# Optimization experiments

Hardware: AMD Instinct MI355X
Metric: run time of the kernel (lower is better)

Reference implementation:

```python
import jax, jax.numpy as jnp
import numpy as np

G = 32            # gridsize
N = G * G         # num_nodes = 1024
F_IN = 32         # input_dim
H = 256           # hidden_dim
L = 4             # n_layers
B = 64            # batch
MID = F_IN + L * H
MIN_VAL = -10000000.0
EPS_LN = 1e-5
EPS_BN = 1e-5


def _grid_edges():
    ids = np.arange(N).reshape(G, G)
    hs, hd = ids[:, :-1].ravel(), ids[:, 1:].ravel()
    vs, vd = ids[:-1, :].ravel(), ids[1:, :].ravel()
    src = np.concatenate([hs, hd, vs, vd]).astype(np.int32)
    dst = np.concatenate([hd, hs, vd, vs]).astype(np.int32)
    return jnp.asarray(src), jnp.asarray(dst)


def setup_inputs() -> dict:
    key = jax.random.key(0)
    ks = jax.random.split(key, 16)
    mask_f = jax.random.bernoulli(ks[0], 0.7, (B, N)).astype(jnp.float32)
    feats = jax.random.normal(ks[1], (B, N * F_IN), dtype=jnp.float32)
    observations = jnp.concatenate([mask_f, feats], axis=1)
    src, dst = _grid_edges()
    def lin(k, fi, fo):
        return jax.random.normal(k, (fi, fo), dtype=jnp.float32) / np.sqrt(fi)
    W0 = lin(ks[2], F_IN, H); b0 = jnp.zeros((H,), jnp.float32)
    g0 = jnp.ones((H,), jnp.float32); be0 = jnp.zeros((H,), jnp.float32)
    Ws = jax.random.normal(ks[3], (L - 1, H, H), jnp.float32) / np.sqrt(H)
    bs = jnp.zeros((L - 1, H), jnp.float32)
    gs = jnp.ones((L - 1, H), jnp.float32); bes = jnp.zeros((L - 1, H), jnp.float32)
    W1 = lin(ks[4], MID, 2 * H); b1 = jnp.zeros((2 * H,), jnp.float32)
    bn_g = jnp.ones((2 * H,), jnp.float32); bn_b = jnp.zeros((2 * H,), jnp.float32)
    bn_m = jax.random.normal(ks[5], (2 * H,), jnp.float32) * 0.1
    bn_v = jax.random.uniform(ks[6], (2 * H,), jnp.float32, 0.5, 1.5)
    W2 = lin(ks[7], 2 * H, 1); b2 = jnp.zeros((1,), jnp.float32)
    return {"observations": observations, "src": src, "dst": dst,
            "W0": W0, "b0": b0, "g0": g0, "be0": be0,
            "Ws": Ws, "bs": bs, "gs": gs, "bes": bes,
            "W1": W1, "b1": b1, "bn_g": bn_g, "bn_b": bn_b,
            "bn_m": bn_m, "bn_v": bn_v, "W2": W2, "b2": b2}


def _layer_norm(z, g, b):
    mu = z.mean(-1, keepdims=True)
    var = z.var(-1, keepdims=True)
    return (z - mu) / jnp.sqrt(var + EPS_LN) * g + b


def reference(observations, src, dst, W0, b0, g0, be0, Ws, bs, gs, bes,
              W1, b1, bn_g, bn_b, bn_m, bn_v, W2, b2):
    mask = observations[:, :N] != 0.0                      # [B,N] bool action mask
    x = observations[:, N:].reshape(B, N, F_IN)            # node features
    outs = [x]
    h = x
    for l in range(L):
        # GIN with eps=-1: (1+eps)*x_i vanishes -> mlp(sum of neighbor features)
        agg = jnp.zeros_like(h).at[:, dst, :].add(h[:, src, :])
        W, bb, g, be = ((W0, b0, g0, be0) if l == 0
                        else (Ws[l - 1], bs[l - 1], gs[l - 1], bes[l - 1]))
        h = jax.nn.relu(_layer_norm(agg @ W + bb, g, be))  # mlp ReLU; outer .relu() is idempotent
        outs.append(h)
    xc = jnp.concatenate(outs, axis=-1).reshape(B * N, MID)
    z = xc @ W1 + b1
    z = (z - bn_m) / jnp.sqrt(bn_v + EPS_BN) * bn_g + bn_b  # BatchNorm1d eval mode
    z = jax.nn.relu(z)                                       # dropout off in eval
    y = (z @ W2 + b2).reshape(B, N)
    return jnp.where(mask, y, MIN_VAL)
```

## Files before the change

kernel.cpp:

```cpp
#include <hip/hip_runtime.h>
#include <stdint.h>

#define FIN 32
#define HD 256
#define MIDK 1056
#define HF 512
#define MROWS 65536
#define OBS_STRIDE 33792

typedef float f32x2 __attribute__((ext_vector_type(2)));
typedef float f32x4 __attribute__((ext_vector_type(4)));


__device__ __forceinline__ unsigned pack4fp8(float a, float b, float c, float d) {
    int w = __builtin_amdgcn_cvt_pk_fp8_f32(a, b, 0, false);
    return (unsigned)__builtin_amdgcn_cvt_pk_fp8_f32(c, d, w, true);
}
__device__ __forceinline__ unsigned char f2fp8(float f) {
    return (unsigned char)(__builtin_amdgcn_cvt_pk_fp8_f32(f, f, 0, false) & 0xff);
}

__device__ __forceinline__ void glds16(const void* g, void* l) {
    __builtin_amdgcn_global_load_lds(
        (const __attribute__((address_space(1))) unsigned int*)g,
        (__attribute__((address_space(3))) unsigned int*)l,
        16, 0, 0);
}

#define WAITV(N) asm volatile("s_waitcnt vmcnt(" #N ")" ::: "memory")
#define WAITLGKM0() asm volatile("s_waitcnt lgkmcnt(0)" ::: "memory")
__device__ __forceinline__ void barx() {
    asm volatile("" ::: "memory");
    __builtin_amdgcn_s_barrier();
    asm volatile("" ::: "memory");
}

__device__ __forceinline__ void gather16(const float* __restrict__ src, int stride, int n,
                                         unsigned char* __restrict__ dst) {
    float f[16];
#pragma unroll
    for (int j = 0; j < 16; ++j) f[j] = src[(size_t)j * stride + n];
    uint4 o;
    o.x = pack4fp8(f[0],  f[1],  f[2],  f[3]);
    o.y = pack4fp8(f[4],  f[5],  f[6],  f[7]);
    o.z = pack4fp8(f[8],  f[9],  f[10], f[11]);
    o.w = pack4fp8(f[12], f[13], f[14], f[15]);
    *(uint4*)dst = o;
}

__global__ __launch_bounds__(256) void k_prep_w(
        const float* __restrict__ W0, const float* __restrict__ Ws,
        const float* __restrict__ W1,
        unsigned char* __restrict__ Wt0, unsigned char* __restrict__ WtL,
        unsigned char* __restrict__ WtF) {
    const int b = blockIdx.x, t = threadIdx.x;
    if (b < 2) {
        int s = b * 256 + t;
        int hh = s >> 8, n = s & 255;
        gather16(W0 + (size_t)(hh * 16) * HD, HD, n, Wt0 + (size_t)s * 16);
    } else if (b < 50) {
        int u = (b - 2) * 256 + t;
        int l = u >> 12, s = u & 4095;
        int kb = s >> 9, hh = (s >> 8) & 1, n = s & 255;
        gather16(Ws + (size_t)l * 65536 + (size_t)(kb * 32 + hh * 16) * HD, HD, n,
                 WtL + (size_t)l * 65536 + (size_t)s * 16);
    } else {
        int s = (b - 50) * 256 + t;
        int kb = s >> 11, hh = (s >> 9) & 3, n = s & 511;
        int k0 = kb * 64 + hh * 16;
        if (k0 < MIDK)
            gather16(W1 + (size_t)k0 * HF, HF, n, WtF + (size_t)s * 16);
        else
            *(uint4*)(WtF + (size_t)s * 16) = make_uint4(0, 0, 0, 0);
    }
}

template <int K>
__global__ __launch_bounds__(256, 4) void k_layer(
        const unsigned char* __restrict__ Hin,
        const float* __restrict__ obs,
        const unsigned char* __restrict__ Wt,
        const float* __restrict__ bias, const float* __restrict__ gamma,
        const float* __restrict__ beta, unsigned char* __restrict__ Hout) {
    constexpr int KB = K / 32;
    __shared__ __align__(16) unsigned char Agg[(K / 16) * 64 * 16];
    __shared__ float ls[64], lss[64];
    const int t = threadIdx.x;
    const int w = t >> 6, lane = t & 63, quad = lane >> 4, l15 = lane & 15;
    const int q1 = quad >> 1, q0 = quad & 1;
    const int m0 = ((blockIdx.x & 7) * 128 + (blockIdx.x >> 3)) * 64;
    const int img = m0 >> 10, node0 = m0 & 1023;
    if (t < 64) { ls[t] = 0.f; lss[t] = 0.f; }

    if constexpr (K == 256) {
        const int r = t & 63, sg = t >> 6;
        const int node = node0 + r;
        const int rr = node >> 5, cc = node & 31;
        const unsigned char* Hb = Hin + (size_t)img * 262144;
#pragma unroll
        for (int p = 0; p < 2; ++p) {
            const int seg = p * 4 + sg;
            float s[32];
#pragma unroll
            for (int i = 0; i < 32; ++i) s[i] = 0.f;
            auto addn = [&](int nn) {
                uint4 u0 = *(const uint4*)(Hb + ((size_t)(2 * seg) * 1024 + nn) * 16);
                uint4 u1 = *(const uint4*)(Hb + ((size_t)(2 * seg + 1) * 1024 + nn) * 16);
                unsigned uu[8] = {u0.x, u0.y, u0.z, u0.w, u1.x, u1.y, u1.z, u1.w};
#pragma unroll
                for (int i = 0; i < 8; ++i) {
                    f32x2 lo = __builtin_amdgcn_cvt_pk_f32_fp8(uu[i], false);
                    f32x2 hi = __builtin_amdgcn_cvt_pk_f32_fp8(uu[i], true);
                    s[4 * i + 0] += lo.x; s[4 * i + 1] += lo.y;
                    s[4 * i + 2] += hi.x; s[4 * i + 3] += hi.y;
                }
            };
            if (cc > 0)  addn(node - 1);
            if (cc < 31) addn(node + 1);
            if (rr > 0)  addn(node - 32);
            if (rr < 31) addn(node + 32);
            unsigned ow[8];
#pragma unroll
            for (int i = 0; i < 8; ++i)
                ow[i] = pack4fp8(s[4 * i], s[4 * i + 1], s[4 * i + 2], s[4 * i + 3]);
            ((uint4*)Agg)[(2 * seg) * 64 + r]     = make_uint4(ow[0], ow[1], ow[2], ow[3]);
            ((uint4*)Agg)[(2 * seg + 1) * 64 + r] = make_uint4(ow[4], ow[5], ow[6], ow[7]);
        }
    } else {
        const int r = t >> 2, seg4 = t & 3;
        const int node = node0 + r;
        const int rr = node >> 5, cc = node & 31;
        const float* fb = obs + (size_t)img * OBS_STRIDE + 1024 + seg4 * 8;
        float s[8] = {0, 0, 0, 0, 0, 0, 0, 0};
        auto addnf = [&](int nn) {
            const float4* fp = (const float4*)(fb + nn * 32);
            float4 f0 = fp[0], f1 = fp[1];
            s[0] += f0.x; s[1] += f0.y; s[2] += f0.z; s[3] += f0.w;
            s[4] += f1.x; s[5] += f1.y; s[6] += f1.z; s[7] += f1.w;
        };
        if (cc > 0)  addnf(node - 1);
        if (cc < 31) addnf(node + 1);
        if (rr > 0)  addnf(node - 32);
        if (rr < 31) addnf(node + 32);
        uint2 o;
        o.x = pack4fp8(s[0], s[1], s[2], s[3]);
        o.y = pack4fp8(s[4], s[5], s[6], s[7]);
        *(uint2*)(Agg + ((seg4 >> 1) * 64 + r) * 16 + (seg4 & 1) * 8) = o;
    }
    __syncthreads();

    f32x4 acc[4][4] = {};
    const unsigned char* bbase = Wt + ((size_t)(q1 * 256 + w * 64 + l15)) * 16 + q0 * 8;
    const unsigned char* abase = Agg + ((size_t)(q1 * 64 + l15)) * 16 + q0 * 8;

#define LOADBL(dst, kb) { const unsigned char* bp = bbase + (size_t)(kb) * 8192; \
    dst[0] = *(const long long*)(bp);        dst[1] = *(const long long*)(bp + 256); \
    dst[2] = *(const long long*)(bp + 512);  dst[3] = *(const long long*)(bp + 768); }
#define MFMAL(buf, kb) { long long af[4]; \
    _Pragma("unroll") for (int mt = 0; mt < 4; ++mt) \
        af[mt] = *(const long long*)(abase + (kb) * 2048 + mt * 256); \
    _Pragma("unroll") for (int mt = 0; mt < 4; ++mt) \
    _Pragma("unroll") for (int nt = 0; nt < 4; ++nt) \
        acc[mt][nt] = __builtin_amdgcn_mfma_f32_16x16x32_fp8_fp8(af[mt], buf[nt], acc[mt][nt], 0, 0, 0); }

    if constexpr (KB == 1) {
        long long bA[4];
        LOADBL(bA, 0);
        MFMAL(bA, 0);
    } else {
        long long bA[4], bB[4];
        LOADBL(bA, 0);
#pragma unroll
        for (int j = 0; j < KB / 2 - 1; ++j) {
            LOADBL(bB, 2 * j + 1);
            MFMAL(bA, 2 * j);
            LOADBL(bA, 2 * j + 2);
            MFMAL(bB, 2 * j + 1);
        }
        LOADBL(bB, KB - 1);
        MFMAL(bA, KB - 2);
        MFMAL(bB, KB - 1);
    }
#undef LOADBL
#undef MFMAL

#pragma unroll
    for (int mt = 0; mt < 4; ++mt) {
        float s0 = 0, s1 = 0, s2 = 0, s3 = 0, u0 = 0, u1 = 0, u2 = 0, u3 = 0;
#pragma unroll
        for (int nt = 0; nt < 4; ++nt) {
            int col = w * 64 + nt * 16 + l15;
            float bv = bias[col];
            f32x4 vv = acc[mt][nt];
            vv.x += bv; vv.y += bv; vv.z += bv; vv.w += bv;
            acc[mt][nt] = vv;
            s0 += vv.x; u0 += vv.x * vv.x;
            s1 += vv.y; u1 += vv.y * vv.y;
            s2 += vv.z; u2 += vv.z * vv.z;
            s3 += vv.w; u3 += vv.w * vv.w;
        }
#pragma unroll
        for (int msk = 1; msk < 16; msk <<= 1) {
            s0 += __shfl_xor(s0, msk); u0 += __shfl_xor(u0, msk);
            s1 += __shfl_xor(s1, msk); u1 += __shfl_xor(u1, msk);
            s2 += __shfl_xor(s2, msk); u2 += __shfl_xor(u2, msk);
            s3 += __shfl_xor(s3, msk); u3 += __shfl_xor(u3, msk);
        }
        if (l15 == 0) {
            int rl = mt * 16 + quad * 4;
            atomicAdd(&ls[rl + 0], s0); atomicAdd(&lss[rl + 0], u0);
            atomicAdd(&ls[rl + 1], s1); atomicAdd(&lss[rl + 1], u1);
            atomicAdd(&ls[rl + 2], s2); atomicAdd(&lss[rl + 2], u2);
            atomicAdd(&ls[rl + 3], s3); atomicAdd(&lss[rl + 3], u3);
        }
    }
    __syncthreads();
#pragma unroll
    for (int mt = 0; mt < 4; ++mt) {
        int rl = mt * 16 + quad * 4;
        float mu0 = ls[rl + 0] * (1.f / 256.f), mu1 = ls[rl + 1] * (1.f / 256.f);
        float mu2 = ls[rl + 2] * (1.f / 256.f), mu3 = ls[rl + 3] * (1.f / 256.f);
        float rs0 = rsqrtf(lss[rl + 0] * (1.f / 256.f) - mu0 * mu0 + 1e-5f);
        float rs1 = rsqrtf(lss[rl + 1] * (1.f / 256.f) - mu1 * mu1 + 1e-5f);
        float rs2 = rsqrtf(lss[rl + 2] * (1.f / 256.f) - mu2 * mu2 + 1e-5f);
        float rs3 = rsqrtf(lss[rl + 3] * (1.f / 256.f) - mu3 * mu3 + 1e-5f);
#pragma unroll
        for (int nt = 0; nt < 4; ++nt) {
            int col = w * 64 + nt * 16 + l15;
            float gg = gamma[col], be = beta[col];
            f32x4 vv = acc[mt][nt];
            size_t rb = ((size_t)(img * 16 + w * 4 + nt) * 1024
                         + node0 + mt * 16 + quad * 4) * 16 + l15;
            Hout[rb]      = f2fp8(fmaxf((vv.x - mu0) * rs0 * gg + be, 0.f));
            Hout[rb + 16] = f2fp8(fmaxf((vv.y - mu1) * rs1 * gg + be, 0.f));
            Hout[rb + 32] = f2fp8(fmaxf((vv.z - mu2) * rs2 * gg + be, 0.f));
            Hout[rb + 48] = f2fp8(fmaxf((vv.w - mu3) * rs3 * gg + be, 0.f));
        }
    }
}

__global__ __launch_bounds__(512) void k_final(
        const unsigned char* __restrict__ h0, const unsigned char* __restrict__ h1,
        const unsigned char* __restrict__ h2, const unsigned char* __restrict__ h3,
        const unsigned char* __restrict__ WtF,
        const float* __restrict__ b1,
        const float* __restrict__ bng, const float* __restrict__ bnb,
        const float* __restrict__ bnm, const float* __restrict__ bnv,
        const float* __restrict__ W2, const float* __restrict__ b2,
        const float* __restrict__ obs, float* __restrict__ out) {
    __shared__ __align__(16) unsigned char As[2][264 * 16];
    __shared__ __align__(16) unsigned char Bsm[2][2056 * 16];
    __shared__ float yred[64];
    const int t = threadIdx.x;
    const int w = t >> 6, lane = t & 63, quad = lane >> 4, l15 = lane & 15;
    const int q1 = quad >> 1, q0 = quad & 1;
    const int wr = w >> 2, wc = w & 3;
    const int m0 = ((blockIdx.x & 7) * 128 + (blockIdx.x >> 3)) * 64;
    const int bimg = m0 >> 10, node0 = m0 & 1023;
    if (t < 64) yred[t] = 0.f;

    const unsigned char* hbuf[4] = {h0, h1, h2, h3};
    f32x4 acc[2][8] = {};

    auto stageB = [&](int it, unsigned char* Bb, int nB) {
#pragma unroll
        for (int i = 0; i < nB; ++i)
            glds16(WtF + ((size_t)it * 2048 + (size_t)i * 512 + t) * 16,
                   Bb + ((size_t)i * 514 + (t & ~63)) * 16);
    };
    auto stageA = [&](int it, unsigned char* Ab, int steps) {
        if (t < steps * 128) {
            int h = t >> 6, r = t & 63;
            int j = it * 64 + h * 16 - FIN;
            glds16(hbuf[j >> 8] + ((size_t)(bimg * 16 + ((j & 255) >> 4)) * 1024 + node0 + r) * 16,
                   Ab + (size_t)h * 66 * 16);
        }
    };
    auto compute = [&](const unsigned char* Ab, const unsigned char* Bb, int steps) {
        for (int s2 = 0; s2 < steps; ++s2) {
            long long af[2], bf[8];
#pragma unroll
            for (int mt = 0; mt < 2; ++mt)
                af[mt] = *(const long long*)(Ab + ((s2 * 2 + q1) * 66 + wr * 32 + mt * 16 + l15) * 16 + q0 * 8);
#pragma unroll
            for (int nt = 0; nt < 8; ++nt)
                bf[nt] = *(const long long*)(Bb + ((size_t)((s2 * 2 + q1) * 514 + wc * 128 + nt * 16 + l15)) * 16 + q0 * 8);
            __builtin_amdgcn_s_setprio(1);
#pragma unroll
            for (int mt = 0; mt < 2; ++mt)
#pragma unroll
                for (int nt = 0; nt < 8; ++nt)
                    acc[mt][nt] = __builtin_amdgcn_mfma_f32_16x16x32_fp8_fp8(af[mt], bf[nt], acc[mt][nt], 0, 0, 0);
            __builtin_amdgcn_s_setprio(0);
        }
    };

    if (t < 128) {
        int h = t >> 6, r = t & 63;
        const float* p = obs + (size_t)bimg * OBS_STRIDE + 1024 + (node0 + r) * 32 + h * 16;
        float4 f0 = *(const float4*)p, f1 = *(const float4*)(p + 4);
        float4 f2 = *(const float4*)(p + 8), f3 = *(const float4*)(p + 12);
        uint4 o;
        o.x = pack4fp8(f0.x, f0.y, f0.z, f0.w);
        o.y = pack4fp8(f1.x, f1.y, f1.z, f1.w);
        o.z = pack4fp8(f2.x, f2.y, f2.z, f2.w);
        o.w = pack4fp8(f3.x, f3.y, f3.z, f3.w);
        *(uint4*)(As[0] + (h * 66 + r) * 16) = o;
    } else if (t < 256) {
        int h = t >> 6, r = t & 63;
        glds16(h0 + ((size_t)(bimg * 16 + (h - 2)) * 1024 + node0 + r) * 16,
               As[0] + (size_t)h * 66 * 16);
    }
    stageB(0, Bsm[0], 4);
    stageA(1, As[1], 2);
    stageB(1, Bsm[1], 4);
    if (w < 4) { WAITV(5); } else { WAITV(4); }
    WAITLGKM0();
    barx();
    compute(As[0], Bsm[0], 2);
    barx();

#pragma unroll 1
    for (int it = 1; it < 17; ++it) {
        const int cur = it & 1;
        if (it < 15) {
            stageA(it + 1, As[cur ^ 1], 2);
            stageB(it + 1, Bsm[cur ^ 1], 4);
            if (w < 4) { WAITV(5); } else { WAITV(4); }
        } else if (it == 15) {
            stageA(16, As[cur ^ 1], 1);
            stageB(16, Bsm[cur ^ 1], 2);
            if (w < 2) { WAITV(3); } else { WAITV(2); }
        } else {
            WAITV(0);
        }
        barx();
        compute(As[cur], Bsm[cur], (it < 16) ? 2 : 1);
        barx();
    }

    float scv[8], sbv[8], w2v[8];
#pragma unroll
    for (int nt = 0; nt < 8; ++nt) {
        int col = wc * 128 + nt * 16 + l15;
        float sc = bng[col] * rsqrtf(bnv[col] + 1e-5f);
        scv[nt] = sc;
        sbv[nt] = (b1[col] - bnm[col]) * sc + bnb[col];
        w2v[nt] = W2[col];
    }
#pragma unroll
    for (int mt = 0; mt < 2; ++mt) {
        float p0 = 0, p1 = 0, p2 = 0, p3 = 0;
#pragma unroll
        for (int nt = 0; nt < 8; ++nt) {
            f32x4 vv = acc[mt][nt];
            p0 += fmaxf(vv.x * scv[nt] + sbv[nt], 0.f) * w2v[nt];
            p1 += fmaxf(vv.y * scv[nt] + sbv[nt], 0.f) * w2v[nt];
            p2 += fmaxf(vv.z * scv[nt] + sbv[nt], 0.f) * w2v[nt];
            p3 += fmaxf(vv.w * scv[nt] + sbv[nt], 0.f) * w2v[nt];
        }
#pragma unroll
        for (int msk = 1; msk < 16; msk <<= 1) {
            p0 += __shfl_xor(p0, msk);
            p1 += __shfl_xor(p1, msk);
            p2 += __shfl_xor(p2, msk);
            p3 += __shfl_xor(p3, msk);
        }
        if (l15 == 0) {
            int rl = wr * 32 + mt * 16 + quad * 4;
            atomicAdd(&yred[rl + 0], p0);
            atomicAdd(&yred[rl + 1], p1);
            atomicAdd(&yred[rl + 2], p2);
            atomicAdd(&yred[rl + 3], p3);
        }
    }
    __syncthreads();
    if (t < 64) {
        int gm = m0 + t;
        float mk = obs[(size_t)bimg * OBS_STRIDE + (node0 + t)];
        out[gm] = (mk != 0.f) ? yred[t] + b2[0] : -10000000.0f;
    }
}

extern "C" void kernel_launch(void* const* d_in, const int* in_sizes, int n_in,
                              void* d_out, int out_size, void* d_ws, size_t ws_size,
                              hipStream_t stream) {
    const float* obs = (const float*)d_in[0];
    const float* W0  = (const float*)d_in[3];
    const float* b0  = (const float*)d_in[4];
    const float* g0  = (const float*)d_in[5];
    const float* be0 = (const float*)d_in[6];
    const float* Ws  = (const float*)d_in[7];
    const float* bs  = (const float*)d_in[8];
    const float* gs  = (const float*)d_in[9];
    const float* bes = (const float*)d_in[10];
    const float* W1  = (const float*)d_in[11];
    const float* b1  = (const float*)d_in[12];
    const float* bng = (const float*)d_in[13];
    const float* bnb = (const float*)d_in[14];
    const float* bnm = (const float*)d_in[15];
    const float* bnv = (const float*)d_in[16];
    const float* W2  = (const float*)d_in[17];
    const float* b2  = (const float*)d_in[18];
    float* out = (float*)d_out;

    char* ws = (char*)d_ws;
    unsigned char* h0  = (unsigned char*)(ws);
    unsigned char* h1  = (unsigned char*)(ws + 16777216);
    unsigned char* h2  = (unsigned char*)(ws + 33554432);
    unsigned char* h3  = (unsigned char*)(ws + 50331648);
    unsigned char* Wt0 = (unsigned char*)(ws + 67108864);
    unsigned char* WtL = (unsigned char*)(ws + 67117056);
    unsigned char* WtF = (unsigned char*)(ws + 67313664);

    k_prep_w<<<182, 256, 0, stream>>>(W0, Ws, W1, Wt0, WtL, WtF);

    k_layer<FIN><<<1024, 256, 0, stream>>>(h0 , obs, Wt0, b0, g0, be0, h0);
    k_layer<HD> <<<1024, 256, 0, stream>>>(h0, obs, WtL,              bs,       gs,       bes,       h1);
    k_layer<HD> <<<1024, 256, 0, stream>>>(h1, obs, WtL + 65536,      bs + 256, gs + 256, bes + 256, h2);
    k_layer<HD> <<<1024, 256, 0, stream>>>(h2, obs, WtL + 2 * 65536,  bs + 512, gs + 512, bes + 512, h3);

    k_final<<<1024, 512, 0, stream>>>(h0, h1, h2, h3, WtF, b1, bng, bnb, bnm, bnv,
                                      W2, b2, obs, out);
}
```

Baseline: 234.3 us.

## Use 16x16x128 scaled FP8 MFMA in final GEMM with 128-wide K stages

Moves the final 1056x512 projection from 16x16x32 fp8 MFMAs to the gfx950 scaled 16x16x128 f8f6f4 MFMA, with neutral scale exponents. The K pipeline now takes 128-wide steps (9 iterations instead of 17). Each wave owns all 64 rows and a 64-column slice instead of a 32x128 tile. The W1 pre-transpose layout and the prep grid size change to match. This cuts instruction issue and loop and barrier overhead, at the cost of larger LDS buffers and padded K (1056 to 1152), which means wasted MFMA work and possible LDS bank conflicts from removing the row padding.

```diff
diff --git a/kernel.cpp b/kernel.cpp
--- a/kernel.cpp
+++ b/kernel.cpp
@@ -10,6 +10,8 @@
 
 typedef float f32x2 __attribute__((ext_vector_type(2)));
 typedef float f32x4 __attribute__((ext_vector_type(4)));
+typedef int   i32x4 __attribute__((ext_vector_type(4)));
+typedef int   i32x8 __attribute__((ext_vector_type(8)));
 
 
 __device__ __forceinline__ unsigned pack4fp8(float a, float b, float c, float d) {
@@ -66,8 +68,9 @@
                  WtL + (size_t)l * 65536 + (size_t)s * 16);
     } else {
         int s = (b - 50) * 256 + t;
-        int kb = s >> 11, hh = (s >> 9) & 3, n = s & 511;
-        int k0 = kb * 64 + hh * 16;
+        int it = s >> 12, r2 = s & 4095;
+        int hh = r2 >> 9, n = r2 & 511;
+        int k0 = it * 128 + hh * 16;
         if (k0 < MIDK)
             gather16(W1 + (size_t)k0 * HF, HF, n, WtF + (size_t)s * 16);
         else
@@ -248,56 +251,61 @@
         const float* __restrict__ bnm, const float* __restrict__ bnv,
         const float* __restrict__ W2, const float* __restrict__ b2,
         const float* __restrict__ obs, float* __restrict__ out) {
-    __shared__ __align__(16) unsigned char As[2][264 * 16];
-    __shared__ __align__(16) unsigned char Bsm[2][2056 * 16];
+    __shared__ __align__(16) unsigned char As[2][8 * 64 * 16];
+    __shared__ __align__(16) unsigned char Bsm[2][8 * 512 * 16];
     __shared__ float yred[64];
     const int t = threadIdx.x;
     const int w = t >> 6, lane = t & 63, quad = lane >> 4, l15 = lane & 15;
-    const int q1 = quad >> 1, q0 = quad & 1;
-    const int wr = w >> 2, wc = w & 3;
     const int m0 = ((blockIdx.x & 7) * 128 + (blockIdx.x >> 3)) * 64;
     const int bimg = m0 >> 10, node0 = m0 & 1023;
     if (t < 64) yred[t] = 0.f;
 
     const unsigned char* hbuf[4] = {h0, h1, h2, h3};
-    f32x4 acc[2][8] = {};
-
-    auto stageB = [&](int it, unsigned char* Bb, int nB) {
-#pragma unroll
-        for (int i = 0; i < nB; ++i)
-            glds16(WtF + ((size_t)it * 2048 + (size_t)i * 512 + t) * 16,
-                   Bb + ((size_t)i * 514 + (t & ~63)) * 16);
+    f32x4 acc[4][4] = {};
+
+    auto stageA = [&](int it, unsigned char* Ab) {
+        int u = it * 8 + w;
+        const unsigned char* src;
+        if (u >= 2 && u < 66) {
+            int j = u - 2;
+            src = hbuf[j >> 4] + ((size_t)(bimg * 16 + (j & 15)) * 1024 + node0) * 16;
+        } else {
+            src = h0 + ((size_t)(bimg * 16) * 1024 + node0) * 16;
+        }
+        glds16(src + (size_t)lane * 16, Ab + (size_t)w * 1024);
     };
-    auto stageA = [&](int it, unsigned char* Ab, int steps) {
-        if (t < steps * 128) {
-            int h = t >> 6, r = t & 63;
-            int j = it * 64 + h * 16 - FIN;
-            glds16(hbuf[j >> 8] + ((size_t)(bimg * 16 + ((j & 255) >> 4)) * 1024 + node0 + r) * 16,
-                   Ab + (size_t)h * 66 * 16);
-        }
+    auto stageB = [&](int it, unsigned char* Bb) {
+#pragma unroll
+        for (int i = 0; i < 8; ++i)
+            glds16(WtF + ((size_t)it * 4096 + i * 512 + t) * 16,
+                   Bb + ((size_t)(i * 512) + (t & ~63)) * 16);
     };
-    auto compute = [&](const unsigned char* Ab, const unsigned char* Bb, int steps) {
-        for (int s2 = 0; s2 < steps; ++s2) {
-            long long af[2], bf[8];
-#pragma unroll
-            for (int mt = 0; mt < 2; ++mt)
-                af[mt] = *(const long long*)(Ab + ((s2 * 2 + q1) * 66 + wr * 32 + mt * 16 + l15) * 16 + q0 * 8);
-#pragma unroll
-            for (int nt = 0; nt < 8; ++nt)
-                bf[nt] = *(const long long*)(Bb + ((size_t)((s2 * 2 + q1) * 514 + wc * 128 + nt * 16 + l15)) * 16 + q0 * 8);
+    auto compute = [&](const unsigned char* Ab, const unsigned char* Bb) {
+        i32x8 bf[4];
+#pragma unroll
+        for (int nt = 0; nt < 4; ++nt) {
+            const unsigned char* bp = Bb + ((size_t)(quad * 2) * 512 + w * 64 + nt * 16 + l15) * 16;
+            i32x4 lo = *(const i32x4*)bp;
+            i32x4 hi = *(const i32x4*)(bp + 512 * 16);
+            bf[nt] = (i32x8){lo[0], lo[1], lo[2], lo[3], hi[0], hi[1], hi[2], hi[3]};
+        }
+#pragma unroll
+        for (int mt = 0; mt < 4; ++mt) {
+            const unsigned char* ap = Ab + ((size_t)(quad * 2) * 64 + mt * 16 + l15) * 16;
+            i32x4 lo = *(const i32x4*)ap;
+            i32x4 hi = *(const i32x4*)(ap + 64 * 16);
+            i32x8 af = (i32x8){lo[0], lo[1], lo[2], lo[3], hi[0], hi[1], hi[2], hi[3]};
             __builtin_amdgcn_s_setprio(1);
 #pragma unroll
-            for (int mt = 0; mt < 2; ++mt)
-#pragma unroll
-                for (int nt = 0; nt < 8; ++nt)
-                    acc[mt][nt] = __builtin_amdgcn_mfma_f32_16x16x32_fp8_fp8(af[mt], bf[nt], acc[mt][nt], 0, 0, 0);
+            for (int nt = 0; nt < 4; ++nt)
+                acc[mt][nt] = __builtin_amdgcn_mfma_scale_f32_16x16x128_f8f6f4(
+                    af, bf[nt], acc[mt][nt], 0, 0, 0, 0x7F7F7F7F, 0, 0x7F7F7F7F);
             __builtin_amdgcn_s_setprio(0);
         }
     };
 
-    if (t < 128) {
-        int h = t >> 6, r = t & 63;
-        const float* p = obs + (size_t)bimg * OBS_STRIDE + 1024 + (node0 + r) * 32 + h * 16;
+    if (w < 2) {
+        const float* p = obs + (size_t)bimg * OBS_STRIDE + 1024 + (size_t)(node0 + lane) * 32 + w * 16;
         float4 f0 = *(const float4*)p, f1 = *(const float4*)(p + 4);
         float4 f2 = *(const float4*)(p + 8), f3 = *(const float4*)(p + 12);
         uint4 o;
@@ -305,54 +313,48 @@
         o.y = pack4fp8(f1.x, f1.y, f1.z, f1.w);
         o.z = pack4fp8(f2.x, f2.y, f2.z, f2.w);
         o.w = pack4fp8(f3.x, f3.y, f3.z, f3.w);
-        *(uint4*)(As[0] + (h * 66 + r) * 16) = o;
-    } else if (t < 256) {
-        int h = t >> 6, r = t & 63;
-        glds16(h0 + ((size_t)(bimg * 16 + (h - 2)) * 1024 + node0 + r) * 16,
-               As[0] + (size_t)h * 66 * 16);
-    }
-    stageB(0, Bsm[0], 4);
-    stageA(1, As[1], 2);
-    stageB(1, Bsm[1], 4);
-    if (w < 4) { WAITV(5); } else { WAITV(4); }
+        *(uint4*)(As[0] + ((size_t)w * 64 + lane) * 16) = o;
+    } else {
+        stageA(0, As[0]);
+    }
+    stageB(0, Bsm[0]);
+    stageA(1, As[1]);
+    stageB(1, Bsm[1]);
+    WAITV(9);
     WAITLGKM0();
     barx();
-    compute(As[0], Bsm[0], 2);
+    compute(As[0], Bsm[0]);
     barx();
 
 #pragma unroll 1
-    for (int it = 1; it < 17; ++it) {
+    for (int it = 1; it < 9; ++it) {
         const int cur = it & 1;
-        if (it < 15) {
-            stageA(it + 1, As[cur ^ 1], 2);
-            stageB(it + 1, Bsm[cur ^ 1], 4);
-            if (w < 4) { WAITV(5); } else { WAITV(4); }
-        } else if (it == 15) {
-            stageA(16, As[cur ^ 1], 1);
-            stageB(16, Bsm[cur ^ 1], 2);
-            if (w < 2) { WAITV(3); } else { WAITV(2); }
+        if (it < 8) {
+            stageA(it + 1, As[cur ^ 1]);
+            stageB(it + 1, Bsm[cur ^ 1]);
+            WAITV(9);
         } else {
             WAITV(0);
         }
         barx();
-        compute(As[cur], Bsm[cur], (it < 16) ? 2 : 1);
+        compute(As[cur], Bsm[cur]);
         barx();
     }
 
-    float scv[8], sbv[8], w2v[8];
-#pragma unroll
-    for (int nt = 0; nt < 8; ++nt) {
-        int col = wc * 128 + nt * 16 + l15;
+    float scv[4], sbv[4], w2v[4];
+#pragma unroll
+    for (int nt = 0; nt < 4; ++nt) {
+        int col = w * 64 + nt * 16 + l15;
         float sc = bng[col] * rsqrtf(bnv[col] + 1e-5f);
         scv[nt] = sc;
         sbv[nt] = (b1[col] - bnm[col]) * sc + bnb[col];
         w2v[nt] = W2[col];
     }
 #pragma unroll
-    for (int mt = 0; mt < 2; ++mt) {
+    for (int mt = 0; mt < 4; ++mt) {
         float p0 = 0, p1 = 0, p2 = 0, p3 = 0;
 #pragma unroll
-        for (int nt = 0; nt < 8; ++nt) {
+        for (int nt = 0; nt < 4; ++nt) {
             f32x4 vv = acc[mt][nt];
             p0 += fmaxf(vv.x * scv[nt] + sbv[nt], 0.f) * w2v[nt];
             p1 += fmaxf(vv.y * scv[nt] + sbv[nt], 0.f) * w2v[nt];
@@ -367,7 +369,7 @@
             p3 += __shfl_xor(p3, msk);
         }
         if (l15 == 0) {
-            int rl = wr * 32 + mt * 16 + quad * 4;
+            int rl = mt * 16 + quad * 4;
             atomicAdd(&yred[rl + 0], p0);
             atomicAdd(&yred[rl + 1], p1);
             atomicAdd(&yred[rl + 2], p2);
@@ -413,7 +415,7 @@
     unsigned char* WtL = (unsigned char*)(ws + 67117056);
     unsigned char* WtF = (unsigned char*)(ws + 67313664);
 
-    k_prep_w<<<182, 256, 0, stream>>>(W0, Ws, W1, Wt0, WtL, WtF);
+    k_prep_w<<<194, 256, 0, stream>>>(W0, Ws, W1, Wt0, WtL, WtF);
 
     k_layer<FIN><<<1024, 256, 0, stream>>>(h0 , obs, Wt0, b0, g0, be0, h0);
     k_layer<HD> <<<1024, 256, 0, stream>>>(h0, obs, WtL,              bs,       gs,       bes,       h1);
```

Result: no change. 237.3 us (+1.3%).
